# Optimization experiments

Measured on AMD Instinct MI355X. Metric: run time of the kernel, lower is better.

## Reference

```python
import jax, jax.numpy as jnp
import numpy as np


def grid_sample_3d(vol, grid):
    """torch F.grid_sample 3D, mode='bilinear' (trilinear), align_corners=True.
    vol:  [B, C, Din, Hin, Win]
    grid: [B, Dout, Hout, Wout, 3] with xyz in [-1, 1] (x->W, y->H, z->D)
    returns [B, C, Dout, Hout, Wout]
    """
    B, C, Din, Hin, Win = vol.shape
    v = jnp.transpose(vol, (0, 2, 3, 4, 1))
    # align_corners=True: -1 -> 0, +1 -> size-1
    ix = (grid[..., 0] + 1.0) * 0.5 * (Win - 1)
    iy = (grid[..., 1] + 1.0) * 0.5 * (Hin - 1)
    iz = (grid[..., 2] + 1.0) * 0.5 * (Din - 1)
    x0 = jnp.floor(ix); y0 = jnp.floor(iy); z0 = jnp.floor(iz)
    wx = (ix - x0)[..., None]
    wy = (iy - y0)[..., None]
    wz = (iz - z0)[..., None]
    x0i = jnp.clip(x0.astype(jnp.int32), 0, Win - 1); x1i = jnp.clip(x0i + 1, 0, Win - 1)
    y0i = jnp.clip(y0.astype(jnp.int32), 0, Hin - 1); y1i = jnp.clip(y0i + 1, 0, Hin - 1)
    z0i = jnp.clip(z0.astype(jnp.int32), 0, Din - 1); z1i = jnp.clip(z0i + 1, 0, Din - 1)
    b = jnp.arange(B)[:, None, None, None]
    g = lambda z, y, x: v[b, z, y, x]  # [B, Dout, Hout, Wout, C]
    # interpolate along x, then y, then z
    c00 = g(z0i, y0i, x0i) * (1.0 - wx) + g(z0i, y0i, x1i) * wx
    c01 = g(z0i, y1i, x0i) * (1.0 - wx) + g(z0i, y1i, x1i) * wx
    c10 = g(z1i, y0i, x0i) * (1.0 - wx) + g(z1i, y0i, x1i) * wx
    c11 = g(z1i, y1i, x0i) * (1.0 - wx) + g(z1i, y1i, x1i) * wx
    c0 = c00 * (1.0 - wy) + c01 * wy
    c1 = c10 * (1.0 - wy) + c11 * wy
    out = c0 * (1.0 - wz) + c1 * wz  # [B, Dout, Hout, Wout, C]
    return jnp.transpose(out, (0, 4, 1, 2, 3))


def setup_inputs() -> dict:
    B, C, G, T = 2, 4, 128, 96
    key = jax.random.key(0)
    k1, k2, k3, k4 = jax.random.split(key, 4)
    grids = jax.random.uniform(k1, (B, G, G, G, 3), jnp.float32, minval=-1.0, maxval=1.0)
    deformation = jax.random.normal(k2, (B, 3, G, G, G), jnp.float32) * 0.1
    correction = jax.random.normal(k3, (B, C, G, G, G), jnp.float32) * 0.05
    template = jax.random.normal(k4, (B, C, T, T, T), jnp.float32)
    return {"grids": grids, "deformation": deformation, "correction": correction, "template": template}


def reference(grids, deformation, correction, template):
    # deformation: [B,3,W,H,D] -> [B,D,H,W,3]
    defp = jnp.transpose(deformation, (0, 4, 3, 2, 1))
    field = jnp.tanh(grids + defp)
    out = grid_sample_3d(template, field)           # [B,C,D,H,W]
    out = jnp.transpose(out, (0, 1, 4, 3, 2)) + correction  # [B,C,W,H,D]
    return (out, defp)
```

## Files before the change

kernel.cpp:

```cpp
#include <hip/hip_runtime.h>
#include <stdint.h>

#define G  128
#define TT 96
#define NB 2
#define NC 4
#define CS (TT * TT * TT)

__global__ __launch_bounds__(256) void tmpl_repack_kernel(
        const float* __restrict__ tmpl, float4* __restrict__ out) {
    const int NV = NB * CS;
    int idx = blockIdx.x * 256 + threadIdx.x;
    if (idx >= NV) return;
    int b = idx / CS;
    int s = idx - b * CS;
    const float* base = tmpl + (size_t)b * NC * CS + s;
    float4 p;
    p.x = base[0];
    p.y = base[CS];
    p.z = base[2 * CS];
    p.w = base[3 * CS];
    out[idx] = p;
}

template <bool PACKED>
__global__ __launch_bounds__(256) void fused_sample_kernel(
        const float* __restrict__ grids,
        const float* __restrict__ deform,
        const float* __restrict__ corr,
        const float4* __restrict__ tmpl_cl,
        const float* __restrict__ tmpl_raw,
        float* __restrict__ out2,
        float* __restrict__ defp) {
    __shared__ float lds_def[3][32][33];
    __shared__ float lds_field[3][32][33];

    int blk = blockIdx.x;
    int wt = blk & 3;
    int dt = (blk >> 2) & 3;
    int h  = (blk >> 4) & 127;
    int b  = blk >> 11;
    int w0 = wt << 5, d0 = dt << 5;
    int tid = threadIdx.x;

    for (int idx = tid; idx < 768; idx += 256) {
        int c   = idx >> 8;
        int rem = idx & 255;
        int i   = rem >> 3;
        int j4  = (rem & 7) << 2;
        size_t off = ((((size_t)b * 3 + c) * G + (w0 + i)) * G + h) * G + (d0 + j4);
        float4 v = *(const float4*)(deform + off);
        lds_def[c][i][j4 + 0] = v.x;
        lds_def[c][i][j4 + 1] = v.y;
        lds_def[c][i][j4 + 2] = v.z;
        lds_def[c][i][j4 + 3] = v.w;
    }
    __syncthreads();

    for (int idx = tid; idx < 768; idx += 256) {
        int j = idx / 24;
        int t = idx - j * 24;
        size_t off = (((((size_t)b * G + (d0 + j)) * G + h) * G + w0) * 3) + (size_t)t * 4;
        float gv[4], dv[4];
        *(float4*)gv = *(const float4*)(grids + off);
#pragma unroll
        for (int k = 0; k < 4; ++k) {
            int e = t * 4 + k;
            int i = e / 3;
            int c = e - 3 * i;
            float d = lds_def[c][i][j];
            lds_field[c][j][i] = tanhf(gv[k] + d);
            dv[k] = d;
        }
        *(float4*)(defp + off) = *(float4*)dv;
    }
    __syncthreads();

    const float SC = 0.5f * (TT - 1);
    for (int p = tid; p < 1024; p += 256) {
        int i = p >> 5;
        int j = p & 31;
        float ix = (lds_field[0][j][i] + 1.0f) * SC;
        float iy = (lds_field[1][j][i] + 1.0f) * SC;
        float iz = (lds_field[2][j][i] + 1.0f) * SC;
        float x0f = floorf(ix), y0f = floorf(iy), z0f = floorf(iz);
        float wx = ix - x0f, wy = iy - y0f, wz = iz - z0f;
        int x0 = min(max((int)x0f, 0), TT - 1);
        int y0 = min(max((int)y0f, 0), TT - 1);
        int z0 = min(max((int)z0f, 0), TT - 1);
        int x1 = min(x0 + 1, TT - 1);
        int y1 = min(y0 + 1, TT - 1);
        int z1 = min(z0 + 1, TT - 1);
        float mx = 1.0f - wx, my = 1.0f - wy, mz = 1.0f - wz;
        float w000 = mx * my * mz, w001 = wx * my * mz;
        float w010 = mx * wy * mz, w011 = wx * wy * mz;
        float w100 = mx * my * wz, w101 = wx * my * wz;
        float w110 = mx * wy * wz, w111 = wx * wy * wz;

        float r0, r1, r2, r3;
        if (PACKED) {
            const float4* tb = tmpl_cl + (size_t)b * CS;
            float4 v000 = tb[((size_t)z0 * TT + y0) * TT + x0];
            float4 v001 = tb[((size_t)z0 * TT + y0) * TT + x1];
            float4 v010 = tb[((size_t)z0 * TT + y1) * TT + x0];
            float4 v011 = tb[((size_t)z0 * TT + y1) * TT + x1];
            float4 v100 = tb[((size_t)z1 * TT + y0) * TT + x0];
            float4 v101 = tb[((size_t)z1 * TT + y0) * TT + x1];
            float4 v110 = tb[((size_t)z1 * TT + y1) * TT + x0];
            float4 v111 = tb[((size_t)z1 * TT + y1) * TT + x1];
            r0 = v000.x*w000 + v001.x*w001 + v010.x*w010 + v011.x*w011
               + v100.x*w100 + v101.x*w101 + v110.x*w110 + v111.x*w111;
            r1 = v000.y*w000 + v001.y*w001 + v010.y*w010 + v011.y*w011
               + v100.y*w100 + v101.y*w101 + v110.y*w110 + v111.y*w111;
            r2 = v000.z*w000 + v001.z*w001 + v010.z*w010 + v011.z*w011
               + v100.z*w100 + v101.z*w101 + v110.z*w110 + v111.z*w111;
            r3 = v000.w*w000 + v001.w*w001 + v010.w*w010 + v011.w*w011
               + v100.w*w100 + v101.w*w101 + v110.w*w110 + v111.w*w111;
        } else {
            size_t i000 = ((size_t)z0 * TT + y0) * TT + x0;
            size_t i001 = ((size_t)z0 * TT + y0) * TT + x1;
            size_t i010 = ((size_t)z0 * TT + y1) * TT + x0;
            size_t i011 = ((size_t)z0 * TT + y1) * TT + x1;
            size_t i100 = ((size_t)z1 * TT + y0) * TT + x0;
            size_t i101 = ((size_t)z1 * TT + y0) * TT + x1;
            size_t i110 = ((size_t)z1 * TT + y1) * TT + x0;
            size_t i111 = ((size_t)z1 * TT + y1) * TT + x1;
            float rr[4];
#pragma unroll
            for (int c = 0; c < NC; ++c) {
                const float* tb = tmpl_raw + ((size_t)b * NC + c) * CS;
                rr[c] = tb[i000]*w000 + tb[i001]*w001 + tb[i010]*w010 + tb[i011]*w011
                      + tb[i100]*w100 + tb[i101]*w101 + tb[i110]*w110 + tb[i111]*w111;
            }
            r0 = rr[0]; r1 = rr[1]; r2 = rr[2]; r3 = rr[3];
        }

        int w = w0 + i, d = d0 + j;
        size_t obase = ((((size_t)b * NC) * (size_t)G + w) * G + h) * G + d;
        const size_t cstride = (size_t)G * G * G;
        out2[obase + 0 * cstride] = r0 + corr[obase + 0 * cstride];
        out2[obase + 1 * cstride] = r1 + corr[obase + 1 * cstride];
        out2[obase + 2 * cstride] = r2 + corr[obase + 2 * cstride];
        out2[obase + 3 * cstride] = r3 + corr[obase + 3 * cstride];
    }
}

extern "C" void kernel_launch(void* const* d_in, const int* in_sizes, int n_in,
                              void* d_out, int out_size, void* d_ws, size_t ws_size,
                              hipStream_t stream) {
    const float* grids  = (const float*)d_in[0];
    const float* deform = (const float*)d_in[1];
    const float* corr   = (const float*)d_in[2];
    const float* tmpl   = (const float*)d_in[3];
    float* out2 = (float*)d_out;
    float* defp = out2 + (size_t)NB * NC * G * G * G;
    float4* tmpl_cl = (float4*)d_ws;

    const size_t ws_needed = (size_t)NB * CS * sizeof(float4);
    const bool packed = (ws_size >= ws_needed);

    if (packed) {
        int nv = NB * CS;
        tmpl_repack_kernel<<<(nv + 255) / 256, 256, 0, stream>>>(tmpl, tmpl_cl);
    }

    int nblk = NB * G * 16;
    if (packed) {
        fused_sample_kernel<true><<<nblk, 256, 0, stream>>>(
            grids, deform, corr, tmpl_cl, tmpl, out2, defp);
    } else {
        fused_sample_kernel<false><<<nblk, 256, 0, stream>>>(
            grids, deform, corr, tmpl_cl, tmpl, out2, defp);
    }
}
```

Before: 407.8 us.

## Repack template as fp16 channel-packed 2x2x2 Morton bricks

The repack kernel now converts the template to half precision, packs all four channels into one 64-bit word, and stores voxels in 2x2x2 bricks so a trilinear neighbourhood tends to fall in the same or adjacent cache lines. The sampling kernel computes brick indices, loads 8-byte words instead of 16-byte float4s, and unpacks them to float before accumulating. This halves the template footprint and gather bandwidth and improves locality of the random gathers. The cost is fp16 rounding of template values, which may break tolerance, plus extra index arithmetic.

```diff
diff --git a/kernel.cpp b/kernel.cpp
--- a/kernel.cpp
+++ b/kernel.cpp
@@ -1,26 +1,53 @@
 #include <hip/hip_runtime.h>
 #include <stdint.h>
 
-#define G  128
-#define TT 96
-#define NB 2
-#define NC 4
-#define CS (TT * TT * TT)
+#define G   128
+#define TT  96
+#define NB  2
+#define NC  4
+#define CS  (TT * TT * TT)
+#define NBK (48 * 48 * 48)
+
+__device__ __forceinline__ uint16_t f2h(float f) {
+    union { uint16_t u; _Float16 h; } v; v.h = (_Float16)f; return v.u;
+}
+__device__ __forceinline__ void unpack4(uint64_t v, float f[4]) {
+    union { uint32_t u; _Float16 h[2]; } a, b;
+    a.u = (uint32_t)v; b.u = (uint32_t)(v >> 32);
+    f[0] = (float)a.h[0]; f[1] = (float)a.h[1];
+    f[2] = (float)b.h[0]; f[3] = (float)b.h[1];
+}
 
 __global__ __launch_bounds__(256) void tmpl_repack_kernel(
-        const float* __restrict__ tmpl, float4* __restrict__ out) {
-    const int NV = NB * CS;
+        const float* __restrict__ tmpl, uint64_t* __restrict__ out) {
     int idx = blockIdx.x * 256 + threadIdx.x;
-    if (idx >= NV) return;
-    int b = idx / CS;
-    int s = idx - b * CS;
-    const float* base = tmpl + (size_t)b * NC * CS + s;
-    float4 p;
-    p.x = base[0];
-    p.y = base[CS];
-    p.z = base[2 * CS];
-    p.w = base[3 * CS];
-    out[idx] = p;
+    if (idx >= NB * NBK) return;
+    int b = idx / NBK;
+    int s = idx - b * NBK;
+    int bz = s / (48 * 48);
+    int r  = s - bz * 48 * 48;
+    int by = r / 48;
+    int bx = r - by * 48;
+    const float* base = tmpl + (size_t)b * NC * CS
+                      + (((size_t)(bz << 1) * TT + (by << 1)) * TT + (bx << 1));
+    uint64_t vox[8];
+#pragma unroll
+    for (int lz = 0; lz < 2; ++lz)
+#pragma unroll
+    for (int ly = 0; ly < 2; ++ly)
+#pragma unroll
+    for (int lx = 0; lx < 2; ++lx) {
+        uint64_t p = 0;
+#pragma unroll
+        for (int c = 0; c < NC; ++c) {
+            float f = base[(size_t)c * CS + (lz * TT + ly) * TT + lx];
+            p |= (uint64_t)f2h(f) << (16 * c);
+        }
+        vox[(lz << 2) | (ly << 1) | lx] = p;
+    }
+    uint64_t* o = out + ((size_t)b * NBK + s) * 8;
+#pragma unroll
+    for (int k = 0; k < 8; ++k) o[k] = vox[k];
 }
 
 template <bool PACKED>
@@ -28,7 +55,7 @@
         const float* __restrict__ grids,
         const float* __restrict__ deform,
         const float* __restrict__ corr,
-        const float4* __restrict__ tmpl_cl,
+        const uint64_t* __restrict__ tmpl_mx,
         const float* __restrict__ tmpl_raw,
         float* __restrict__ out2,
         float* __restrict__ defp) {
@@ -97,25 +124,47 @@
         float w100 = mx * my * wz, w101 = wx * my * wz;
         float w110 = mx * wy * wz, w111 = wx * wy * wz;
 
-        float r0, r1, r2, r3;
+        float r[4] = {0.f, 0.f, 0.f, 0.f};
         if (PACKED) {
-            const float4* tb = tmpl_cl + (size_t)b * CS;
-            float4 v000 = tb[((size_t)z0 * TT + y0) * TT + x0];
-            float4 v001 = tb[((size_t)z0 * TT + y0) * TT + x1];
-            float4 v010 = tb[((size_t)z0 * TT + y1) * TT + x0];
-            float4 v011 = tb[((size_t)z0 * TT + y1) * TT + x1];
-            float4 v100 = tb[((size_t)z1 * TT + y0) * TT + x0];
-            float4 v101 = tb[((size_t)z1 * TT + y0) * TT + x1];
-            float4 v110 = tb[((size_t)z1 * TT + y1) * TT + x0];
-            float4 v111 = tb[((size_t)z1 * TT + y1) * TT + x1];
-            r0 = v000.x*w000 + v001.x*w001 + v010.x*w010 + v011.x*w011
-               + v100.x*w100 + v101.x*w101 + v110.x*w110 + v111.x*w111;
-            r1 = v000.y*w000 + v001.y*w001 + v010.y*w010 + v011.y*w011
-               + v100.y*w100 + v101.y*w101 + v110.y*w110 + v111.y*w111;
-            r2 = v000.z*w000 + v001.z*w001 + v010.z*w010 + v011.z*w011
-               + v100.z*w100 + v101.z*w101 + v110.z*w110 + v111.z*w111;
-            r3 = v000.w*w000 + v001.w*w001 + v010.w*w010 + v011.w*w011
-               + v100.w*w100 + v101.w*w101 + v110.w*w110 + v111.w*w111;
+            const uint64_t* tb = tmpl_mx + (size_t)b * CS;
+            int bx0 = x0 >> 1, bx1 = x1 >> 1, lx0 = x0 & 1, lx1 = x1 & 1;
+            int by0 = y0 >> 1, by1 = y1 >> 1, ly0 = (y0 & 1) << 1, ly1 = (y1 & 1) << 1;
+            int bz0 = z0 >> 1, bz1 = z1 >> 1, lz0 = (z0 & 1) << 2, lz1 = (z1 & 1) << 2;
+            int rz0y0 = (bz0 * 48 + by0) * 48, rz0y1 = (bz0 * 48 + by1) * 48;
+            int rz1y0 = (bz1 * 48 + by0) * 48, rz1y1 = (bz1 * 48 + by1) * 48;
+            uint64_t v000 = tb[(size_t)((rz0y0 + bx0) << 3) + (lz0 | ly0 | lx0)];
+            uint64_t v001 = tb[(size_t)((rz0y0 + bx1) << 3) + (lz0 | ly0 | lx1)];
+            uint64_t v010 = tb[(size_t)((rz0y1 + bx0) << 3) + (lz0 | ly1 | lx0)];
+            uint64_t v011 = tb[(size_t)((rz0y1 + bx1) << 3) + (lz0 | ly1 | lx1)];
+            uint64_t v100 = tb[(size_t)((rz1y0 + bx0) << 3) + (lz1 | ly0 | lx0)];
+            uint64_t v101 = tb[(size_t)((rz1y0 + bx1) << 3) + (lz1 | ly0 | lx1)];
+            uint64_t v110 = tb[(size_t)((rz1y1 + bx0) << 3) + (lz1 | ly1 | lx0)];
+            uint64_t v111 = tb[(size_t)((rz1y1 + bx1) << 3) + (lz1 | ly1 | lx1)];
+            float f[4];
+            unpack4(v000, f);
+#pragma unroll
+            for (int c = 0; c < 4; ++c) r[c] += f[c] * w000;
+            unpack4(v001, f);
+#pragma unroll
+            for (int c = 0; c < 4; ++c) r[c] += f[c] * w001;
+            unpack4(v010, f);
+#pragma unroll
+            for (int c = 0; c < 4; ++c) r[c] += f[c] * w010;
+            unpack4(v011, f);
+#pragma unroll
+            for (int c = 0; c < 4; ++c) r[c] += f[c] * w011;
+            unpack4(v100, f);
+#pragma unroll
+            for (int c = 0; c < 4; ++c) r[c] += f[c] * w100;
+            unpack4(v101, f);
+#pragma unroll
+            for (int c = 0; c < 4; ++c) r[c] += f[c] * w101;
+            unpack4(v110, f);
+#pragma unroll
+            for (int c = 0; c < 4; ++c) r[c] += f[c] * w110;
+            unpack4(v111, f);
+#pragma unroll
+            for (int c = 0; c < 4; ++c) r[c] += f[c] * w111;
         } else {
             size_t i000 = ((size_t)z0 * TT + y0) * TT + x0;
             size_t i001 = ((size_t)z0 * TT + y0) * TT + x1;
@@ -125,23 +174,22 @@
             size_t i101 = ((size_t)z1 * TT + y0) * TT + x1;
             size_t i110 = ((size_t)z1 * TT + y1) * TT + x0;
             size_t i111 = ((size_t)z1 * TT + y1) * TT + x1;
-            float rr[4];
 #pragma unroll
             for (int c = 0; c < NC; ++c) {
                 const float* tb = tmpl_raw + ((size_t)b * NC + c) * CS;
-                rr[c] = tb[i000]*w000 + tb[i001]*w001 + tb[i010]*w010 + tb[i011]*w011
-                      + tb[i100]*w100 + tb[i101]*w101 + tb[i110]*w110 + tb[i111]*w111;
+                r[c] = tb[i000]*w000 + tb[i001]*w001 + tb[i010]*w010 + tb[i011]*w011
+                     + tb[i100]*w100 + tb[i101]*w101 + tb[i110]*w110 + tb[i111]*w111;
             }
-            r0 = rr[0]; r1 = rr[1]; r2 = rr[2]; r3 = rr[3];
         }
 
         int w = w0 + i, d = d0 + j;
         size_t obase = ((((size_t)b * NC) * (size_t)G + w) * G + h) * G + d;
         const size_t cstride = (size_t)G * G * G;
-        out2[obase + 0 * cstride] = r0 + corr[obase + 0 * cstride];
-        out2[obase + 1 * cstride] = r1 + corr[obase + 1 * cstride];
-        out2[obase + 2 * cstride] = r2 + corr[obase + 2 * cstride];
-        out2[obase + 3 * cstride] = r3 + corr[obase + 3 * cstride];
+#pragma unroll
+        for (int c = 0; c < NC; ++c) {
+            size_t oidx = obase + c * cstride;
+            out2[oidx] = r[c] + corr[oidx];
+        }
     }
 }
 
@@ -154,22 +202,22 @@
     const float* tmpl   = (const float*)d_in[3];
     float* out2 = (float*)d_out;
     float* defp = out2 + (size_t)NB * NC * G * G * G;
-    float4* tmpl_cl = (float4*)d_ws;
-
-    const size_t ws_needed = (size_t)NB * CS * sizeof(float4);
+    uint64_t* tmpl_mx = (uint64_t*)d_ws;
+
+    const size_t ws_needed = (size_t)NB * CS * sizeof(uint64_t);
     const bool packed = (ws_size >= ws_needed);
 
     if (packed) {
-        int nv = NB * CS;
-        tmpl_repack_kernel<<<(nv + 255) / 256, 256, 0, stream>>>(tmpl, tmpl_cl);
+        int nthr = NB * NBK;
+        tmpl_repack_kernel<<<(nthr + 255) / 256, 256, 0, stream>>>(tmpl, tmpl_mx);
     }
 
     int nblk = NB * G * 16;
     if (packed) {
         fused_sample_kernel<true><<<nblk, 256, 0, stream>>>(
-            grids, deform, corr, tmpl_cl, tmpl, out2, defp);
+            grids, deform, corr, tmpl_mx, tmpl, out2, defp);
     } else {
         fused_sample_kernel<false><<<nblk, 256, 0, stream>>>(
-            grids, deform, corr, tmpl_cl, tmpl, out2, defp);
-    }
-}
+            grids, deform, corr, tmpl_mx, tmpl, out2, defp);
+    }
+}
```

Measured after the change: 420.5 us. +3.1%, slower.
